# Optimization experiments

Hardware: AMD Instinct MI355X
Metric: run time of the kernel (lower is better)

The kernel has to match this reference:

```python
import jax, jax.numpy as jnp
import numpy as np

DIM = 256
NUM_HEADS = 8
WINDOW = 7


def setup_inputs() -> dict:
    key = jax.random.key(0)
    ks = jax.random.split(key, 6)
    B, N, C = 4, 2048, DIM
    x = jax.random.normal(ks[0], (B, N, C), dtype=jnp.float32)
    qkv_w = jax.random.normal(ks[1], (3 * C, C), dtype=jnp.float32) * 0.02
    qkv_b = jax.random.normal(ks[2], (3 * C,), dtype=jnp.float32) * 0.02
    proj_w = jax.random.normal(ks[3], (C, C), dtype=jnp.float32) * 0.02
    proj_b = jax.random.normal(ks[4], (C,), dtype=jnp.float32) * 0.02
    bias_table = jax.random.normal(ks[5], ((2 * WINDOW - 1) * NUM_HEADS,), dtype=jnp.float32) * 0.02
    return {"x": x, "qkv_w": qkv_w, "qkv_b": qkv_b, "proj_w": proj_w,
            "proj_b": proj_b, "bias_table": bias_table}


def _rel_bias(bias_table, seq_len):
    w = WINDOW
    coords = jnp.arange(w)
    idx = coords[:, None] - coords[None, :] + (w - 1)  # (w, w), values in [0, 2w-2]
    # Faithful to original: table[idx.view(-1)].view(w,w,-1) -> last dim 1,
    # i.e. bias is shared across heads.
    bias = bias_table[idx]  # (w, w)
    if seq_len <= w:
        return bias[:seq_len, :seq_len]
    repeats = (seq_len + w - 1) // w
    bias = jnp.tile(bias, (repeats, repeats))[:seq_len, :seq_len]
    return bias  # (N, N)


def reference(x, qkv_w, qkv_b, proj_w, proj_b, bias_table):
    B, N, C = x.shape
    H, hd = NUM_HEADS, C // NUM_HEADS
    qkv = x @ qkv_w.T + qkv_b                       # (B, N, 3C)
    qkv = qkv.reshape(B, N, 3, H, hd).transpose(2, 0, 3, 1, 4)
    q, k, v = qkv[0], qkv[1], qkv[2]                # each (B, H, N, hd)
    scale = hd ** -0.5
    attn = jnp.einsum('bhnd,bhmd->bhnm', q, k) * scale  # (B, H, N, N)
    bias = _rel_bias(bias_table, N)                 # (N, N), shared across heads
    attn = attn + bias[None, None, :, :]
    attn = jax.nn.softmax(attn, axis=-1)
    out = jnp.einsum('bhnm,bhmd->bhnd', attn, v)    # (B, H, N, hd)
    out = out.transpose(0, 2, 1, 3).reshape(B, N, C)
    return out @ proj_w.T + proj_b
```

## Files before the change

kernel.cpp:

```cpp
#include <hip/hip_runtime.h>
#include <stdint.h>

#define DIMC   256
#define NHEADS 8
#define HD     32
#define BATCH  4
#define SEQ    2048
#define MTOT   (BATCH * SEQ)
#define QKVN   (MTOT * HD * NHEADS)
#define SCALE  0.17677669529663687f
#define LOG2E  1.4426950408889634f
#define SCL2E  (SCALE * LOG2E)

typedef short bf16x8 __attribute__((ext_vector_type(8)));
typedef float f32x4  __attribute__((ext_vector_type(4)));

#if defined(__has_builtin)
#if __has_builtin(__builtin_amdgcn_exp2f)
#define EXP2F __builtin_amdgcn_exp2f
#else
#define EXP2F exp2f
#endif
#else
#define EXP2F exp2f
#endif

static __device__ __forceinline__ unsigned short f2bf(float f) {
    unsigned int u = __float_as_uint(f);
    u += 0x7fffu + ((u >> 16) & 1u);
    return (unsigned short)(u >> 16);
}

static __device__ __forceinline__ unsigned int cvt2(float a, float b) {
#if defined(__has_builtin) && __has_builtin(__builtin_amdgcn_cvt_pk_bf16_f32)
    typedef __bf16 bf2 __attribute__((ext_vector_type(2)));
    bf2 v = __builtin_amdgcn_cvt_pk_bf16_f32(a, b);
    return __builtin_bit_cast(unsigned int, v);
#else
    return (unsigned int)f2bf(a) | ((unsigned int)f2bf(b) << 16);
#endif
}

static __device__ __forceinline__ bf16x8 ld8f_bf(const float* p) {
    float4 a0 = *(const float4*)p;
    float4 a1 = *(const float4*)(p + 4);
    uint4 pk;
    pk.x = cvt2(a0.x, a0.y); pk.y = cvt2(a0.z, a0.w);
    pk.z = cvt2(a1.x, a1.y); pk.w = cvt2(a1.z, a1.w);
    return __builtin_bit_cast(bf16x8, pk);
}

__global__ __launch_bounds__(256) void gemm_qkv_kernel(
    const float* __restrict__ A,
    const float* __restrict__ W,
    const float* __restrict__ bias,
    unsigned short* __restrict__ qb,
    unsigned short* __restrict__ kb,
    unsigned short* __restrict__ vtb)
{
    __shared__ __align__(16) unsigned short FW[8][64][32];

    const int t    = threadIdx.x;
    const int wave = t >> 6;
    const int lane = t & 63;
    const int cg   = lane & 15;
    const int quad = lane >> 4;
    const int m0   = blockIdx.y * 128;
    const int n0   = blockIdx.x * 64;

    {
        int r  = t >> 2, cb = t & 3;
        int pc = (cb ^ ((r >> 1) & 3)) << 3;
        #pragma unroll
        for (int chunk = 0; chunk < 8; chunk++)
            *(bf16x8*)&FW[chunk][r][pc] =
                ld8f_bf(W + (size_t)(n0 + r) * 256 + chunk * 32 + cb * 8);
    }
    __syncthreads();

    const float* Arow = A + (size_t)(m0 + wave * 16 + cg) * 256 + quad * 8;
    const int rsw = ((cg >> 1) & 3);

    f32x4 acc[2][4];
    #pragma unroll
    for (int s = 0; s < 2; s++)
        #pragma unroll
        for (int c = 0; c < 4; c++) acc[s][c] = (f32x4){0.f, 0.f, 0.f, 0.f};

    #pragma unroll
    for (int chunk = 0; chunk < 8; chunk++) {
        bf16x8 wf[4];
        #pragma unroll
        for (int c = 0; c < 4; c++)
            wf[c] = *(const bf16x8*)&FW[chunk][c * 16 + cg][(quad ^ rsw) << 3];
        #pragma unroll
        for (int s = 0; s < 2; s++) {
            bf16x8 af = ld8f_bf(Arow + (size_t)s * 64 * 256 + chunk * 32);
            #pragma unroll
            for (int c = 0; c < 4; c++)
                acc[s][c] = __builtin_amdgcn_mfma_f32_16x16x32_bf16(af, wf[c], acc[s][c], 0, 0, 0);
        }
    }

    if (blockIdx.x >= 8) {
        float (*TR)[68] = (float (*)[68])(void*)&FW[0][0][0];
        #pragma unroll
        for (int s = 0; s < 2; s++) {
            __syncthreads();
            #pragma unroll
            for (int c = 0; c < 4; c++) {
                int l = c * 16 + cg;
                float bv = bias[n0 + l];
                float4 vv;
                vv.x = acc[s][c][0] + bv; vv.y = acc[s][c][1] + bv;
                vv.z = acc[s][c][2] + bv; vv.w = acc[s][c][3] + bv;
                *(float4*)__builtin_assume_aligned(&TR[l][wave * 16 + quad * 4], 16) = vv;
            }
            __syncthreads();
            int l  = t >> 2;
            int mm = (t & 3) << 4;
            int n  = n0 + l;
            int h  = (n >> 5) & 7;
            int d  = n & 31;
            int b_ = m0 >> 11;
            int nn = (m0 & 2047) + s * 64 + mm;
            const float* tr = (const float*)__builtin_assume_aligned(&TR[l][mm], 16);
            float4 v0 = *(const float4*)(tr);
            float4 v1 = *(const float4*)(tr + 4);
            float4 v2 = *(const float4*)(tr + 8);
            float4 v3 = *(const float4*)(tr + 12);
            uint4 pk0, pk1;
            pk0.x = cvt2(v0.x, v0.y); pk0.y = cvt2(v0.z, v0.w);
            pk0.z = cvt2(v1.x, v1.y); pk0.w = cvt2(v1.z, v1.w);
            pk1.x = cvt2(v2.x, v2.y); pk1.y = cvt2(v2.z, v2.w);
            pk1.z = cvt2(v3.x, v3.y); pk1.w = cvt2(v3.z, v3.w);
            unsigned short* dst = vtb + ((size_t)((b_ * NHEADS + h) * HD + d)) * SEQ + nn;
            *(uint4*)dst       = pk0;
            *(uint4*)(dst + 8) = pk1;
        }
        return;
    }

    #pragma unroll
    for (int s = 0; s < 2; s++) {
        #pragma unroll
        for (int c = 0; c < 4; c++) {
            int n = n0 + c * 16 + cg;
            float bv = bias[n];
            int which = n >> 8;
            int h     = (n >> 5) & 7;
            int d     = n & 31;
            #pragma unroll
            for (int rr = 0; rr < 4; rr++) {
                int m = m0 + s * 64 + wave * 16 + quad * 4 + rr;
                float val = acc[s][c][rr] + bv;
                int b_ = m >> 11;
                int nn = m & 2047;
                int bh = b_ * NHEADS + h;
                if (which == 0)
                    qb[((size_t)bh * SEQ + nn) * HD + d] = f2bf(val * SCL2E);
                else
                    kb[((size_t)bh * SEQ + nn) * HD + d] = f2bf(val);
            }
        }
    }
}

__global__ __launch_bounds__(256) void gemm_proj_kernel(
    const unsigned short* __restrict__ A,
    const float* __restrict__ W,
    const float* __restrict__ bias,
    float* __restrict__ outf)
{
    __shared__ __align__(16) unsigned short FW[8][64][32];

    const int t    = threadIdx.x;
    const int wave = t >> 6;
    const int lane = t & 63;
    const int cg   = lane & 15;
    const int quad = lane >> 4;
    const int m0   = blockIdx.y * 64;
    const int n0   = blockIdx.x * 64;

    {
        int r  = t >> 2, cb = t & 3;
        int pc = (cb ^ ((r >> 1) & 3)) << 3;
        #pragma unroll
        for (int chunk = 0; chunk < 8; chunk++)
            *(bf16x8*)&FW[chunk][r][pc] =
                ld8f_bf(W + (size_t)(n0 + r) * 256 + chunk * 32 + cb * 8);
    }
    __syncthreads();

    const unsigned short* Arow = A + (size_t)(m0 + wave * 16 + cg) * 256 + quad * 8;
    const int rsw = ((cg >> 1) & 3);

    f32x4 acc[4];
    #pragma unroll
    for (int c = 0; c < 4; c++) acc[c] = (f32x4){0.f, 0.f, 0.f, 0.f};

    #pragma unroll
    for (int chunk = 0; chunk < 8; chunk++) {
        bf16x8 af = *(const bf16x8*)(Arow + chunk * 32);
        bf16x8 wf[4];
        #pragma unroll
        for (int c = 0; c < 4; c++)
            wf[c] = *(const bf16x8*)&FW[chunk][c * 16 + cg][(quad ^ rsw) << 3];
        #pragma unroll
        for (int c = 0; c < 4; c++)
            acc[c] = __builtin_amdgcn_mfma_f32_16x16x32_bf16(af, wf[c], acc[c], 0, 0, 0);
    }

    #pragma unroll
    for (int c = 0; c < 4; c++) {
        int n = n0 + c * 16 + cg;
        float bv = bias[n];
        #pragma unroll
        for (int rr = 0; rr < 4; rr++) {
            int m = m0 + wave * 16 + quad * 4 + rr;
            outf[(size_t)m * 256 + n] = acc[c][rr] + bv;
        }
    }
}

__global__ __launch_bounds__(256) void attn_mfma_kernel(
    const unsigned short* __restrict__ Q,
    const unsigned short* __restrict__ K,
    const unsigned short* __restrict__ Vt,
    const float* __restrict__ table,
    unsigned short* __restrict__ AO)
{
    __shared__ __align__(16) unsigned short PL[4][64][72];
    __shared__ __align__(16) unsigned short KA7[7][32];

    const int t    = threadIdx.x;
    const int wave = t >> 6;
    const int lane = t & 63;
    const int cg   = lane & 15;
    const int quad = lane >> 4;

    const int bid = blockIdx.x;
    const int qt  = bid & 31;
    const int bh  = bid >> 5;
    const int b   = bh >> 3;
    const int h   = bh & 7;
    const int q0  = qt * 64;

    if (t < 224) {
        int r = t >> 5, c = t & 31;
        float v = (c < 7) ? table[c - r + 6] * LOG2E : 0.f;
        KA7[r][c] = f2bf(v);
    }
    __syncthreads();

    const unsigned short* Kbase = K  + (size_t)bh * (SEQ * HD);
    const unsigned short* Vbase = Vt + (size_t)bh * (SEQ * HD);

    bf16x8 qf[4], qfa[4];
    #pragma unroll
    for (int qi = 0; qi < 4; qi++) {
        qf[qi]  = *(const bf16x8*)(Q + (size_t)bh * (SEQ * HD) +
                                   (size_t)(q0 + qi * 16 + cg) * HD + quad * 8);
        int p = (q0 + qi * 16 + cg) % 7;
        #pragma unroll
        for (int i = 0; i < 8; i++)
            qfa[qi][i] = (quad == 0 && i == p) ? (short)0x3F80 : (short)0;
    }

    bf16x8 ones;
    #pragma unroll
    for (int i = 0; i < 8; i++) ones[i] = (short)0x3F80;

    f32x4 o[4][2], ol[4];
    #pragma unroll
    for (int qi = 0; qi < 4; qi++) {
        o[qi][0] = (f32x4){0.f, 0.f, 0.f, 0.f};
        o[qi][1] = (f32x4){0.f, 0.f, 0.f, 0.f};
        ol[qi]   = (f32x4){0.f, 0.f, 0.f, 0.f};
    }

    const int kstart = wave * (SEQ / 4);
    int kb7[4];
    #pragma unroll
    for (int jt = 0; jt < 4; jt++) kb7[jt] = (kstart + jt * 16 + cg) % 7;

    #pragma unroll 2
    for (int jj = 0; jj < SEQ / 4; jj += 64) {
        const int j0 = kstart + jj;

        bf16x8 kf[4], kfa[4];
        #pragma unroll
        for (int jt = 0; jt < 4; jt++) {
            kf[jt]  = *(const bf16x8*)(Kbase + (size_t)(j0 + jt * 16 + cg) * HD + quad * 8);
            kfa[jt] = *(const bf16x8*)&KA7[kb7[jt]][quad * 8];
        }
        bf16x8 vf[2][2];
        #pragma unroll
        for (int kt = 0; kt < 2; kt++)
            #pragma unroll
            for (int dt = 0; dt < 2; dt++)
                vf[kt][dt] = *(const bf16x8*)(Vbase + (size_t)(dt * 16 + cg) * SEQ +
                                              j0 + kt * 32 + quad * 8);

        #pragma unroll
        for (int half = 0; half < 2; half++) {
            f32x4 s[2][4];
            #pragma unroll
            for (int qh = 0; qh < 2; qh++) {
                int qi = half * 2 + qh;
                #pragma unroll
                for (int jt = 0; jt < 4; jt++) {
                    s[qh][jt] = __builtin_amdgcn_mfma_f32_16x16x32_bf16(
                        kfa[jt], qfa[qi], (f32x4){0.f, 0.f, 0.f, 0.f}, 0, 0, 0);
                    s[qh][jt] = __builtin_amdgcn_mfma_f32_16x16x32_bf16(
                        kf[jt], qf[qi], s[qh][jt], 0, 0, 0);
                }
            }
            #pragma unroll
            for (int qh = 0; qh < 2; qh++) {
                int qi = half * 2 + qh;
                #pragma unroll
                for (int jt = 0; jt < 4; jt++) {
                    float p0 = EXP2F(s[qh][jt][0]);
                    float p1 = EXP2F(s[qh][jt][1]);
                    float p2 = EXP2F(s[qh][jt][2]);
                    float p3 = EXP2F(s[qh][jt][3]);
                    uint2 w;
                    w.x = cvt2(p0, p1);
                    w.y = cvt2(p2, p3);
                    *(uint2*)&PL[wave][qi * 16 + cg][jt * 16 + quad * 4] = w;
                }
            }
        }
        __builtin_amdgcn_s_waitcnt(0xC07F);

        #pragma unroll
        for (int qi = 0; qi < 4; qi++) {
            bf16x8 pa0 = *(const bf16x8*)&PL[wave][qi * 16 + cg][quad * 8];
            bf16x8 pa1 = *(const bf16x8*)&PL[wave][qi * 16 + cg][32 + quad * 8];
            o[qi][0] = __builtin_amdgcn_mfma_f32_16x16x32_bf16(pa0, vf[0][0], o[qi][0], 0, 0, 0);
            o[qi][0] = __builtin_amdgcn_mfma_f32_16x16x32_bf16(pa1, vf[1][0], o[qi][0], 0, 0, 0);
            o[qi][1] = __builtin_amdgcn_mfma_f32_16x16x32_bf16(pa0, vf[0][1], o[qi][1], 0, 0, 0);
            o[qi][1] = __builtin_amdgcn_mfma_f32_16x16x32_bf16(pa1, vf[1][1], o[qi][1], 0, 0, 0);
            ol[qi]   = __builtin_amdgcn_mfma_f32_16x16x32_bf16(pa0, ones, ol[qi], 0, 0, 0);
            ol[qi]   = __builtin_amdgcn_mfma_f32_16x16x32_bf16(pa1, ones, ol[qi], 0, 0, 0);
        }

        #pragma unroll
        for (int jt = 0; jt < 4; jt++)
            kb7[jt] = (kb7[jt] == 6) ? 0 : kb7[jt] + 1;
    }

    __builtin_amdgcn_s_waitcnt(0xC07F);
    float* OPw = (float*)&PL[wave][0][0];
    #pragma unroll
    for (int qi = 0; qi < 4; qi++) {
        #pragma unroll
        for (int dt = 0; dt < 2; dt++)
            #pragma unroll
            for (int rr = 0; rr < 4; rr++)
                OPw[(qi * 16 + quad * 4 + rr) * 33 + dt * 16 + cg] = o[qi][dt][rr];
        if (cg == 0) {
            #pragma unroll
            for (int rr = 0; rr < 4; rr++)
                OPw[(qi * 16 + quad * 4 + rr) * 33 + 32] = ol[qi][rr];
        }
    }
    __syncthreads();

    {
        int q  = t >> 2;
        int d0 = (t & 3) << 3;
        float l = 0.f;
        float ov[8];
        #pragma unroll
        for (int i = 0; i < 8; i++) ov[i] = 0.f;
        #pragma unroll
        for (int w = 0; w < 4; w++) {
            const float* OPx = (const float*)&PL[w][0][0];
            l += OPx[q * 33 + 32];
            #pragma unroll
            for (int i = 0; i < 8; i++) ov[i] += OPx[q * 33 + d0 + i];
        }
        float inv = 1.f / l;
        unsigned short pk[8];
        #pragma unroll
        for (int i = 0; i < 8; i += 2) {
            unsigned int u = cvt2(ov[i] * inv, ov[i + 1] * inv);
            pk[i]     = (unsigned short)(u & 0xffffu);
            pk[i + 1] = (unsigned short)(u >> 16);
        }
        *(uint4*)(AO + ((size_t)(b * SEQ + q0 + q)) * DIMC + h * HD + d0) = *(const uint4*)pk;
    }
}

extern "C" void kernel_launch(void* const* d_in, const int* in_sizes, int n_in,
                              void* d_out, int out_size, void* d_ws, size_t ws_size,
                              hipStream_t stream) {
    const float* x      = (const float*)d_in[0];
    const float* qkv_w  = (const float*)d_in[1];
    const float* qkv_b  = (const float*)d_in[2];
    const float* proj_w = (const float*)d_in[3];
    const float* proj_b = (const float*)d_in[4];
    const float* table  = (const float*)d_in[5];
    float* out = (float*)d_out;

    unsigned short* ws   = (unsigned short*)d_ws;
    unsigned short* qb   = ws;
    unsigned short* kb   = qb  + (size_t)QKVN;
    unsigned short* vtb  = kb  + (size_t)QKVN;
    unsigned short* ao   = vtb + (size_t)QKVN;

    gemm_qkv_kernel<<<dim3(768 / 64, MTOT / 128), 256, 0, stream>>>(
        x, qkv_w, qkv_b, qb, kb, vtb);

    attn_mfma_kernel<<<dim3(BATCH * NHEADS * (SEQ / 64)), 256, 0, stream>>>(
        qb, kb, vtb, table, ao);

    gemm_proj_kernel<<<dim3(256 / 64, MTOT / 64), 256, 0, stream>>>(
        ao, proj_w, proj_b, out);
}
```

Before: 130.9 us.

## Widen GEMM tiles to 256 output columns per block for A reuse

Both the QKV and projection GEMMs now compute 256 output columns per block instead of 64. Each A row tile is loaded and converted once per block, rather than once per 64-column slice, which cuts redundant fp32 A reads and bf16 conversions. The cost is 128 KB of shared memory for the weight tile, a much larger accumulator register footprint, and far fewer blocks (192 and 128), which lowers occupancy and parallelism on a 256-CU device.

```diff
diff --git a/kernel.cpp b/kernel.cpp
--- a/kernel.cpp
+++ b/kernel.cpp
@@ -58,72 +58,103 @@
     unsigned short* __restrict__ kb,
     unsigned short* __restrict__ vtb)
 {
-    __shared__ __align__(16) unsigned short FW[8][64][32];
+    __shared__ __align__(16) unsigned short FW[4][8][64][32];
 
     const int t    = threadIdx.x;
     const int wave = t >> 6;
     const int lane = t & 63;
     const int cg   = lane & 15;
     const int quad = lane >> 4;
+    const int sup  = blockIdx.x;
     const int m0   = blockIdx.y * 128;
-    const int n0   = blockIdx.x * 64;
+    const int nb   = sup * 256;
 
     {
         int r  = t >> 2, cb = t & 3;
         int pc = (cb ^ ((r >> 1) & 3)) << 3;
         #pragma unroll
-        for (int chunk = 0; chunk < 8; chunk++)
-            *(bf16x8*)&FW[chunk][r][pc] =
-                ld8f_bf(W + (size_t)(n0 + r) * 256 + chunk * 32 + cb * 8);
+        for (int nt = 0; nt < 4; nt++)
+            #pragma unroll
+            for (int chunk = 0; chunk < 8; chunk++)
+                *(bf16x8*)&FW[nt][chunk][r][pc] =
+                    ld8f_bf(W + (size_t)(nb + nt * 64 + r) * 256 + chunk * 32 + cb * 8);
     }
     __syncthreads();
 
     const float* Arow = A + (size_t)(m0 + wave * 16 + cg) * 256 + quad * 8;
     const int rsw = ((cg >> 1) & 3);
 
-    f32x4 acc[2][4];
+    f32x4 acc[2][4][4];
     #pragma unroll
     for (int s = 0; s < 2; s++)
         #pragma unroll
-        for (int c = 0; c < 4; c++) acc[s][c] = (f32x4){0.f, 0.f, 0.f, 0.f};
+        for (int nt = 0; nt < 4; nt++)
+            #pragma unroll
+            for (int c = 0; c < 4; c++) acc[s][nt][c] = (f32x4){0.f, 0.f, 0.f, 0.f};
 
     #pragma unroll
     for (int chunk = 0; chunk < 8; chunk++) {
-        bf16x8 wf[4];
-        #pragma unroll
-        for (int c = 0; c < 4; c++)
-            wf[c] = *(const bf16x8*)&FW[chunk][c * 16 + cg][(quad ^ rsw) << 3];
-        #pragma unroll
-        for (int s = 0; s < 2; s++) {
-            bf16x8 af = ld8f_bf(Arow + (size_t)s * 64 * 256 + chunk * 32);
-            #pragma unroll
-            for (int c = 0; c < 4; c++)
-                acc[s][c] = __builtin_amdgcn_mfma_f32_16x16x32_bf16(af, wf[c], acc[s][c], 0, 0, 0);
-        }
-    }
-
-    if (blockIdx.x >= 8) {
-        float (*TR)[68] = (float (*)[68])(void*)&FW[0][0][0];
+        bf16x8 af[2];
+        #pragma unroll
+        for (int s = 0; s < 2; s++)
+            af[s] = ld8f_bf(Arow + (size_t)s * 64 * 256 + chunk * 32);
+        #pragma unroll
+        for (int nt = 0; nt < 4; nt++)
+            #pragma unroll
+            for (int c = 0; c < 4; c++) {
+                bf16x8 wf = *(const bf16x8*)&FW[nt][chunk][c * 16 + cg][(quad ^ rsw) << 3];
+                #pragma unroll
+                for (int s = 0; s < 2; s++)
+                    acc[s][nt][c] = __builtin_amdgcn_mfma_f32_16x16x32_bf16(
+                        af[s], wf, acc[s][nt][c], 0, 0, 0);
+            }
+    }
+
+    if (sup < 2) {
+        unsigned short* dstb = (sup == 0) ? qb : kb;
+        float scl = (sup == 0) ? SCL2E : 1.0f;
+        #pragma unroll
+        for (int s = 0; s < 2; s++)
+            #pragma unroll
+            for (int nt = 0; nt < 4; nt++)
+                #pragma unroll
+                for (int c = 0; c < 4; c++) {
+                    int nl = nt * 64 + c * 16 + cg;
+                    float bv = bias[nb + nl];
+                    int h = nl >> 5, d = nl & 31;
+                    #pragma unroll
+                    for (int rr = 0; rr < 4; rr++) {
+                        int m  = m0 + s * 64 + wave * 16 + quad * 4 + rr;
+                        int b_ = m >> 11, nn = m & 2047;
+                        dstb[((size_t)(b_ * NHEADS + h) * SEQ + nn) * HD + d] =
+                            f2bf((acc[s][nt][c][rr] + bv) * scl);
+                    }
+                }
+        return;
+    }
+
+    float (*TR)[68] = (float (*)[68])(void*)&FW[0][0][0][0];
+    #pragma unroll
+    for (int nt = 0; nt < 4; nt++) {
         #pragma unroll
         for (int s = 0; s < 2; s++) {
             __syncthreads();
             #pragma unroll
             for (int c = 0; c < 4; c++) {
                 int l = c * 16 + cg;
-                float bv = bias[n0 + l];
+                float bv = bias[nb + nt * 64 + l];
                 float4 vv;
-                vv.x = acc[s][c][0] + bv; vv.y = acc[s][c][1] + bv;
-                vv.z = acc[s][c][2] + bv; vv.w = acc[s][c][3] + bv;
+                vv.x = acc[s][nt][c][0] + bv; vv.y = acc[s][nt][c][1] + bv;
+                vv.z = acc[s][nt][c][2] + bv; vv.w = acc[s][nt][c][3] + bv;
                 *(float4*)__builtin_assume_aligned(&TR[l][wave * 16 + quad * 4], 16) = vv;
             }
             __syncthreads();
             int l  = t >> 2;
             int mm = (t & 3) << 4;
-            int n  = n0 + l;
-            int h  = (n >> 5) & 7;
-            int d  = n & 31;
-            int b_ = m0 >> 11;
-            int nn = (m0 & 2047) + s * 64 + mm;
+            int nl = nt * 64 + l;
+            int h  = nl >> 5, d = nl & 31;
+            int m  = m0 + s * 64 + mm;
+            int b_ = m >> 11, nn = m & 2047;
             const float* tr = (const float*)__builtin_assume_aligned(&TR[l][mm], 16);
             float4 v0 = *(const float4*)(tr);
             float4 v1 = *(const float4*)(tr + 4);
@@ -138,31 +169,6 @@
             *(uint4*)dst       = pk0;
             *(uint4*)(dst + 8) = pk1;
         }
-        return;
-    }
-
-    #pragma unroll
-    for (int s = 0; s < 2; s++) {
-        #pragma unroll
-        for (int c = 0; c < 4; c++) {
-            int n = n0 + c * 16 + cg;
-            float bv = bias[n];
-            int which = n >> 8;
-            int h     = (n >> 5) & 7;
-            int d     = n & 31;
-            #pragma unroll
-            for (int rr = 0; rr < 4; rr++) {
-                int m = m0 + s * 64 + wave * 16 + quad * 4 + rr;
-                float val = acc[s][c][rr] + bv;
-                int b_ = m >> 11;
-                int nn = m & 2047;
-                int bh = b_ * NHEADS + h;
-                if (which == 0)
-                    qb[((size_t)bh * SEQ + nn) * HD + d] = f2bf(val * SCL2E);
-                else
-                    kb[((size_t)bh * SEQ + nn) * HD + d] = f2bf(val);
-            }
-        }
     }
 }
 
@@ -172,7 +178,7 @@
     const float* __restrict__ bias,
     float* __restrict__ outf)
 {
-    __shared__ __align__(16) unsigned short FW[8][64][32];
+    __shared__ __align__(16) unsigned short FW[4][8][64][32];
 
     const int t    = threadIdx.x;
     const int wave = t >> 6;
@@ -180,47 +186,52 @@
     const int cg   = lane & 15;
     const int quad = lane >> 4;
     const int m0   = blockIdx.y * 64;
-    const int n0   = blockIdx.x * 64;
 
     {
         int r  = t >> 2, cb = t & 3;
         int pc = (cb ^ ((r >> 1) & 3)) << 3;
         #pragma unroll
-        for (int chunk = 0; chunk < 8; chunk++)
-            *(bf16x8*)&FW[chunk][r][pc] =
-                ld8f_bf(W + (size_t)(n0 + r) * 256 + chunk * 32 + cb * 8);
+        for (int nt = 0; nt < 4; nt++)
+            #pragma unroll
+            for (int chunk = 0; chunk < 8; chunk++)
+                *(bf16x8*)&FW[nt][chunk][r][pc] =
+                    ld8f_bf(W + (size_t)(nt * 64 + r) * 256 + chunk * 32 + cb * 8);
     }
     __syncthreads();
 
     const unsigned short* Arow = A + (size_t)(m0 + wave * 16 + cg) * 256 + quad * 8;
     const int rsw = ((cg >> 1) & 3);
 
-    f32x4 acc[4];
-    #pragma unroll
-    for (int c = 0; c < 4; c++) acc[c] = (f32x4){0.f, 0.f, 0.f, 0.f};
+    f32x4 acc[4][4];
+    #pragma unroll
+    for (int nt = 0; nt < 4; nt++)
+        #pragma unroll
+        for (int c = 0; c < 4; c++) acc[nt][c] = (f32x4){0.f, 0.f, 0.f, 0.f};
 
     #pragma unroll
     for (int chunk = 0; chunk < 8; chunk++) {
         bf16x8 af = *(const bf16x8*)(Arow + chunk * 32);
-        bf16x8 wf[4];
-        #pragma unroll
-        for (int c = 0; c < 4; c++)
-            wf[c] = *(const bf16x8*)&FW[chunk][c * 16 + cg][(quad ^ rsw) << 3];
-        #pragma unroll
-        for (int c = 0; c < 4; c++)
-            acc[c] = __builtin_amdgcn_mfma_f32_16x16x32_bf16(af, wf[c], acc[c], 0, 0, 0);
-    }
-
-    #pragma unroll
-    for (int c = 0; c < 4; c++) {
-        int n = n0 + c * 16 + cg;
-        float bv = bias[n];
-        #pragma unroll
-        for (int rr = 0; rr < 4; rr++) {
-            int m = m0 + wave * 16 + quad * 4 + rr;
-            outf[(size_t)m * 256 + n] = acc[c][rr] + bv;
-        }
-    }
+        #pragma unroll
+        for (int nt = 0; nt < 4; nt++)
+            #pragma unroll
+            for (int c = 0; c < 4; c++) {
+                bf16x8 wf = *(const bf16x8*)&FW[nt][chunk][c * 16 + cg][(quad ^ rsw) << 3];
+                acc[nt][c] = __builtin_amdgcn_mfma_f32_16x16x32_bf16(af, wf, acc[nt][c], 0, 0, 0);
+            }
+    }
+
+    #pragma unroll
+    for (int nt = 0; nt < 4; nt++)
+        #pragma unroll
+        for (int c = 0; c < 4; c++) {
+            int n = nt * 64 + c * 16 + cg;
+            float bv = bias[n];
+            #pragma unroll
+            for (int rr = 0; rr < 4; rr++) {
+                int m = m0 + wave * 16 + quad * 4 + rr;
+                outf[(size_t)m * 256 + n] = acc[nt][c][rr] + bv;
+            }
+        }
 }
 
 __global__ __launch_bounds__(256) void attn_mfma_kernel(
@@ -411,12 +422,12 @@
     unsigned short* vtb  = kb  + (size_t)QKVN;
     unsigned short* ao   = vtb + (size_t)QKVN;
 
-    gemm_qkv_kernel<<<dim3(768 / 64, MTOT / 128), 256, 0, stream>>>(
+    gemm_qkv_kernel<<<dim3(3, 64), 256, 0, stream>>>(
         x, qkv_w, qkv_b, qb, kb, vtb);
 
     attn_mfma_kernel<<<dim3(BATCH * NHEADS * (SEQ / 64)), 256, 0, stream>>>(
         qb, kb, vtb, table, ao);
 
-    gemm_proj_kernel<<<dim3(256 / 64, MTOT / 64), 256, 0, stream>>>(
+    gemm_proj_kernel<<<dim3(1, 128), 256, 0, stream>>>(
         ao, proj_w, proj_b, out);
 }
```

After: 136.1 us. 4.0% more time.

## Shrink shared memory footprints in GEMM and attention kernels for occupancy

Applied to the files above, without the earlier changes.

The QKV and projection GEMMs now stage the weight tile in two halves of four K-chunks each, halving their weight LDS buffer at the cost of an extra barrier per block. The attention kernel shrinks its per-wave P buffer to 32 rows with an XOR swizzle instead of padding, runs the PV MFMAs after each half rather than once per tile, and does the cross-wave reduction in two passes of 32 rows. The aim is lower LDS use per block so more blocks fit per CU, traded against extra synchronization and more waitcnt stalls between the softmax and PV stages.

```diff
diff --git a/kernel.cpp b/kernel.cpp
--- a/kernel.cpp
+++ b/kernel.cpp
@@ -58,7 +58,9 @@
     unsigned short* __restrict__ kb,
     unsigned short* __restrict__ vtb)
 {
-    __shared__ __align__(16) unsigned short FW[8][64][32];
+    __shared__ __align__(16) unsigned char SM[17408];
+    unsigned short (*FW)[64][32] = (unsigned short (*)[64][32])SM;
+    float (*TR)[68] = (float (*)[68])SM;
 
     const int t    = threadIdx.x;
     const int wave = t >> 6;
@@ -68,16 +70,6 @@
     const int m0   = blockIdx.y * 128;
     const int n0   = blockIdx.x * 64;
 
-    {
-        int r  = t >> 2, cb = t & 3;
-        int pc = (cb ^ ((r >> 1) & 3)) << 3;
-        #pragma unroll
-        for (int chunk = 0; chunk < 8; chunk++)
-            *(bf16x8*)&FW[chunk][r][pc] =
-                ld8f_bf(W + (size_t)(n0 + r) * 256 + chunk * 32 + cb * 8);
-    }
-    __syncthreads();
-
     const float* Arow = A + (size_t)(m0 + wave * 16 + cg) * 256 + quad * 8;
     const int rsw = ((cg >> 1) & 3);
 
@@ -88,22 +80,36 @@
         for (int c = 0; c < 4; c++) acc[s][c] = (f32x4){0.f, 0.f, 0.f, 0.f};
 
     #pragma unroll
-    for (int chunk = 0; chunk < 8; chunk++) {
-        bf16x8 wf[4];
-        #pragma unroll
-        for (int c = 0; c < 4; c++)
-            wf[c] = *(const bf16x8*)&FW[chunk][c * 16 + cg][(quad ^ rsw) << 3];
-        #pragma unroll
-        for (int s = 0; s < 2; s++) {
-            bf16x8 af = ld8f_bf(Arow + (size_t)s * 64 * 256 + chunk * 32);
+    for (int half = 0; half < 2; half++) {
+        if (half) __syncthreads();
+        {
+            int r  = t >> 2, cb = t & 3;
+            int pc = (cb ^ ((r >> 1) & 3)) << 3;
+            #pragma unroll
+            for (int c4 = 0; c4 < 4; c4++)
+                *(bf16x8*)&FW[c4][r][pc] =
+                    ld8f_bf(W + (size_t)(n0 + r) * 256 + (half * 4 + c4) * 32 + cb * 8);
+        }
+        __syncthreads();
+
+        #pragma unroll
+        for (int c4 = 0; c4 < 4; c4++) {
+            int chunk = half * 4 + c4;
+            bf16x8 wf[4];
             #pragma unroll
             for (int c = 0; c < 4; c++)
-                acc[s][c] = __builtin_amdgcn_mfma_f32_16x16x32_bf16(af, wf[c], acc[s][c], 0, 0, 0);
+                wf[c] = *(const bf16x8*)&FW[c4][c * 16 + cg][(quad ^ rsw) << 3];
+            #pragma unroll
+            for (int s = 0; s < 2; s++) {
+                bf16x8 af = ld8f_bf(Arow + (size_t)s * 64 * 256 + chunk * 32);
+                #pragma unroll
+                for (int c = 0; c < 4; c++)
+                    acc[s][c] = __builtin_amdgcn_mfma_f32_16x16x32_bf16(af, wf[c], acc[s][c], 0, 0, 0);
+            }
         }
     }
 
     if (blockIdx.x >= 8) {
-        float (*TR)[68] = (float (*)[68])(void*)&FW[0][0][0];
         #pragma unroll
         for (int s = 0; s < 2; s++) {
             __syncthreads();
@@ -172,7 +178,7 @@
     const float* __restrict__ bias,
     float* __restrict__ outf)
 {
-    __shared__ __align__(16) unsigned short FW[8][64][32];
+    __shared__ __align__(16) unsigned short FW[4][64][32];
 
     const int t    = threadIdx.x;
     const int wave = t >> 6;
@@ -182,16 +188,6 @@
     const int m0   = blockIdx.y * 64;
     const int n0   = blockIdx.x * 64;
 
-    {
-        int r  = t >> 2, cb = t & 3;
-        int pc = (cb ^ ((r >> 1) & 3)) << 3;
-        #pragma unroll
-        for (int chunk = 0; chunk < 8; chunk++)
-            *(bf16x8*)&FW[chunk][r][pc] =
-                ld8f_bf(W + (size_t)(n0 + r) * 256 + chunk * 32 + cb * 8);
-    }
-    __syncthreads();
-
     const unsigned short* Arow = A + (size_t)(m0 + wave * 16 + cg) * 256 + quad * 8;
     const int rsw = ((cg >> 1) & 3);
 
@@ -200,15 +196,30 @@
     for (int c = 0; c < 4; c++) acc[c] = (f32x4){0.f, 0.f, 0.f, 0.f};
 
     #pragma unroll
-    for (int chunk = 0; chunk < 8; chunk++) {
-        bf16x8 af = *(const bf16x8*)(Arow + chunk * 32);
-        bf16x8 wf[4];
-        #pragma unroll
-        for (int c = 0; c < 4; c++)
-            wf[c] = *(const bf16x8*)&FW[chunk][c * 16 + cg][(quad ^ rsw) << 3];
-        #pragma unroll
-        for (int c = 0; c < 4; c++)
-            acc[c] = __builtin_amdgcn_mfma_f32_16x16x32_bf16(af, wf[c], acc[c], 0, 0, 0);
+    for (int half = 0; half < 2; half++) {
+        if (half) __syncthreads();
+        {
+            int r  = t >> 2, cb = t & 3;
+            int pc = (cb ^ ((r >> 1) & 3)) << 3;
+            #pragma unroll
+            for (int c4 = 0; c4 < 4; c4++)
+                *(bf16x8*)&FW[c4][r][pc] =
+                    ld8f_bf(W + (size_t)(n0 + r) * 256 + (half * 4 + c4) * 32 + cb * 8);
+        }
+        __syncthreads();
+
+        #pragma unroll
+        for (int c4 = 0; c4 < 4; c4++) {
+            int chunk = half * 4 + c4;
+            bf16x8 af = *(const bf16x8*)(Arow + chunk * 32);
+            bf16x8 wf[4];
+            #pragma unroll
+            for (int c = 0; c < 4; c++)
+                wf[c] = *(const bf16x8*)&FW[c4][c * 16 + cg][(quad ^ rsw) << 3];
+            #pragma unroll
+            for (int c = 0; c < 4; c++)
+                acc[c] = __builtin_amdgcn_mfma_f32_16x16x32_bf16(af, wf[c], acc[c], 0, 0, 0);
+        }
     }
 
     #pragma unroll
@@ -230,7 +241,7 @@
     const float* __restrict__ table,
     unsigned short* __restrict__ AO)
 {
-    __shared__ __align__(16) unsigned short PL[4][64][72];
+    __shared__ __align__(16) unsigned char SMEM[4][4224];
     __shared__ __align__(16) unsigned short KA7[7][32];
 
     const int t    = threadIdx.x;
@@ -255,6 +266,8 @@
 
     const unsigned short* Kbase = K  + (size_t)bh * (SEQ * HD);
     const unsigned short* Vbase = Vt + (size_t)bh * (SEQ * HD);
+    unsigned short* Pw = (unsigned short*)&SMEM[wave][0];
+    const int csw = cg & 7;
 
     bf16x8 qf[4], qfa[4];
     #pragma unroll
@@ -318,7 +331,6 @@
             }
             #pragma unroll
             for (int qh = 0; qh < 2; qh++) {
-                int qi = half * 2 + qh;
                 #pragma unroll
                 for (int jt = 0; jt < 4; jt++) {
                     float p0 = EXP2F(s[qh][jt][0]);
@@ -328,22 +340,24 @@
                     uint2 w;
                     w.x = cvt2(p0, p1);
                     w.y = cvt2(p2, p3);
-                    *(uint2*)&PL[wave][qi * 16 + cg][jt * 16 + quad * 4] = w;
+                    int pc = (2 * jt + (quad >> 1)) ^ csw;
+                    *(uint2*)(Pw + (qh * 16 + cg) * 64 + pc * 8 + (quad & 1) * 4) = w;
                 }
             }
-        }
-        __builtin_amdgcn_s_waitcnt(0xC07F);
-
-        #pragma unroll
-        for (int qi = 0; qi < 4; qi++) {
-            bf16x8 pa0 = *(const bf16x8*)&PL[wave][qi * 16 + cg][quad * 8];
-            bf16x8 pa1 = *(const bf16x8*)&PL[wave][qi * 16 + cg][32 + quad * 8];
-            o[qi][0] = __builtin_amdgcn_mfma_f32_16x16x32_bf16(pa0, vf[0][0], o[qi][0], 0, 0, 0);
-            o[qi][0] = __builtin_amdgcn_mfma_f32_16x16x32_bf16(pa1, vf[1][0], o[qi][0], 0, 0, 0);
-            o[qi][1] = __builtin_amdgcn_mfma_f32_16x16x32_bf16(pa0, vf[0][1], o[qi][1], 0, 0, 0);
-            o[qi][1] = __builtin_amdgcn_mfma_f32_16x16x32_bf16(pa1, vf[1][1], o[qi][1], 0, 0, 0);
-            ol[qi]   = __builtin_amdgcn_mfma_f32_16x16x32_bf16(pa0, ones, ol[qi], 0, 0, 0);
-            ol[qi]   = __builtin_amdgcn_mfma_f32_16x16x32_bf16(pa1, ones, ol[qi], 0, 0, 0);
+            __builtin_amdgcn_s_waitcnt(0xC07F);
+
+            #pragma unroll
+            for (int qh = 0; qh < 2; qh++) {
+                int qi = half * 2 + qh;
+                bf16x8 pa0 = *(const bf16x8*)(Pw + (qh * 16 + cg) * 64 + ((quad ^ csw) << 3));
+                bf16x8 pa1 = *(const bf16x8*)(Pw + (qh * 16 + cg) * 64 + (((4 + quad) ^ csw) << 3));
+                o[qi][0] = __builtin_amdgcn_mfma_f32_16x16x32_bf16(pa0, vf[0][0], o[qi][0], 0, 0, 0);
+                o[qi][0] = __builtin_amdgcn_mfma_f32_16x16x32_bf16(pa1, vf[1][0], o[qi][0], 0, 0, 0);
+                o[qi][1] = __builtin_amdgcn_mfma_f32_16x16x32_bf16(pa0, vf[0][1], o[qi][1], 0, 0, 0);
+                o[qi][1] = __builtin_amdgcn_mfma_f32_16x16x32_bf16(pa1, vf[1][1], o[qi][1], 0, 0, 0);
+                ol[qi]   = __builtin_amdgcn_mfma_f32_16x16x32_bf16(pa0, ones, ol[qi], 0, 0, 0);
+                ol[qi]   = __builtin_amdgcn_mfma_f32_16x16x32_bf16(pa1, ones, ol[qi], 0, 0, 0);
+            }
         }
 
         #pragma unroll
@@ -351,46 +365,41 @@
             kb7[jt] = (kb7[jt] == 6) ? 0 : kb7[jt] + 1;
     }
 
-    __builtin_amdgcn_s_waitcnt(0xC07F);
-    float* OPw = (float*)&PL[wave][0][0];
-    #pragma unroll
-    for (int qi = 0; qi < 4; qi++) {
-        #pragma unroll
-        for (int dt = 0; dt < 2; dt++)
-            #pragma unroll
-            for (int rr = 0; rr < 4; rr++)
-                OPw[(qi * 16 + quad * 4 + rr) * 33 + dt * 16 + cg] = o[qi][dt][rr];
-        if (cg == 0) {
-            #pragma unroll
-            for (int rr = 0; rr < 4; rr++)
-                OPw[(qi * 16 + quad * 4 + rr) * 33 + 32] = ol[qi][rr];
-        }
-    }
-    __syncthreads();
-
-    {
-        int q  = t >> 2;
-        int d0 = (t & 3) << 3;
+    #pragma unroll
+    for (int p = 0; p < 2; p++) {
+        __syncthreads();
+        float* OPw = (float*)&SMEM[wave][0];
+        #pragma unroll
+        for (int qh = 0; qh < 2; qh++) {
+            int qi = p * 2 + qh;
+            #pragma unroll
+            for (int dt = 0; dt < 2; dt++)
+                #pragma unroll
+                for (int rr = 0; rr < 4; rr++)
+                    OPw[(qh * 16 + quad * 4 + rr) * 33 + dt * 16 + cg] = o[qi][dt][rr];
+            if (cg == 0) {
+                #pragma unroll
+                for (int rr = 0; rr < 4; rr++)
+                    OPw[(qh * 16 + quad * 4 + rr) * 33 + 32] = ol[qi][rr];
+            }
+        }
+        __syncthreads();
+        int ql = t >> 3;
+        int d0 = (t & 7) << 2;
         float l = 0.f;
-        float ov[8];
-        #pragma unroll
-        for (int i = 0; i < 8; i++) ov[i] = 0.f;
+        float ov[4] = {0.f, 0.f, 0.f, 0.f};
         #pragma unroll
         for (int w = 0; w < 4; w++) {
-            const float* OPx = (const float*)&PL[w][0][0];
-            l += OPx[q * 33 + 32];
-            #pragma unroll
-            for (int i = 0; i < 8; i++) ov[i] += OPx[q * 33 + d0 + i];
+            const float* OPx = (const float*)&SMEM[w][0];
+            l += OPx[ql * 33 + 32];
+            #pragma unroll
+            for (int i = 0; i < 4; i++) ov[i] += OPx[ql * 33 + d0 + i];
         }
         float inv = 1.f / l;
-        unsigned short pk[8];
-        #pragma unroll
-        for (int i = 0; i < 8; i += 2) {
-            unsigned int u = cvt2(ov[i] * inv, ov[i + 1] * inv);
-            pk[i]     = (unsigned short)(u & 0xffffu);
-            pk[i + 1] = (unsigned short)(u >> 16);
-        }
-        *(uint4*)(AO + ((size_t)(b * SEQ + q0 + q)) * DIMC + h * HD + d0) = *(const uint4*)pk;
+        uint2 pk;
+        pk.x = cvt2(ov[0] * inv, ov[1] * inv);
+        pk.y = cvt2(ov[2] * inv, ov[3] * inv);
+        *(uint2*)(AO + ((size_t)(b * SEQ + q0 + p * 32 + ql)) * DIMC + h * HD + d0) = pk;
     }
 }
 
@@ -411,12 +420,12 @@
     unsigned short* vtb  = kb  + (size_t)QKVN;
     unsigned short* ao   = vtb + (size_t)QKVN;
 
-    gemm_qkv_kernel<<<dim3(768 / 64, MTOT / 128), 256, 0, stream>>>(
+    gemm_qkv_kernel<<<dim3(12, 64), 256, 0, stream>>>(
         x, qkv_w, qkv_b, qb, kb, vtb);
 
     attn_mfma_kernel<<<dim3(BATCH * NHEADS * (SEQ / 64)), 256, 0, stream>>>(
         qb, kb, vtb, table, ao);
 
-    gemm_proj_kernel<<<dim3(256 / 64, MTOT / 64), 256, 0, stream>>>(
+    gemm_proj_kernel<<<dim3(4, 128), 256, 0, stream>>>(
         ao, proj_w, proj_b, out);
 }
```

New measurement: 154.2 us. 1.18x slower.

## Hold weight fragments in registers and drop LDS staging in both GEMMs

Applied to the files above, without the earlier changes.

Both projection GEMMs stop staging the weight tile in shared memory. Each wave instead keeps its 16 output columns' weight fragments in registers for the whole K=256 and reuses them across 128 rows, loading A fragments straight from global. The V transpose now writes packed uint2 directly instead of going through an LDS transpose. The proj kernel processes 128 rows per block, so the grid is halved, and the KA7 LDS row is padded to 40. This removes LDS traffic and barriers but increases redundant global A loads per block, since each wave re-reads all A rows, and raises register pressure.

```diff
diff --git a/kernel.cpp b/kernel.cpp
--- a/kernel.cpp
+++ b/kernel.cpp
@@ -58,109 +58,70 @@
     unsigned short* __restrict__ kb,
     unsigned short* __restrict__ vtb)
 {
-    __shared__ __align__(16) unsigned short FW[8][64][32];
-
     const int t    = threadIdx.x;
     const int wave = t >> 6;
     const int lane = t & 63;
     const int cg   = lane & 15;
     const int quad = lane >> 4;
-    const int m0   = blockIdx.y * 128;
     const int n0   = blockIdx.x * 64;
-
-    {
-        int r  = t >> 2, cb = t & 3;
-        int pc = (cb ^ ((r >> 1) & 3)) << 3;
-        #pragma unroll
-        for (int chunk = 0; chunk < 8; chunk++)
-            *(bf16x8*)&FW[chunk][r][pc] =
-                ld8f_bf(W + (size_t)(n0 + r) * 256 + chunk * 32 + cb * 8);
-    }
-    __syncthreads();
-
-    const float* Arow = A + (size_t)(m0 + wave * 16 + cg) * 256 + quad * 8;
-    const int rsw = ((cg >> 1) & 3);
-
-    f32x4 acc[2][4];
-    #pragma unroll
-    for (int s = 0; s < 2; s++)
-        #pragma unroll
-        for (int c = 0; c < 4; c++) acc[s][c] = (f32x4){0.f, 0.f, 0.f, 0.f};
-
-    #pragma unroll
-    for (int chunk = 0; chunk < 8; chunk++) {
-        bf16x8 wf[4];
-        #pragma unroll
-        for (int c = 0; c < 4; c++)
-            wf[c] = *(const bf16x8*)&FW[chunk][c * 16 + cg][(quad ^ rsw) << 3];
-        #pragma unroll
-        for (int s = 0; s < 2; s++) {
-            bf16x8 af = ld8f_bf(Arow + (size_t)s * 64 * 256 + chunk * 32);
-            #pragma unroll
-            for (int c = 0; c < 4; c++)
-                acc[s][c] = __builtin_amdgcn_mfma_f32_16x16x32_bf16(af, wf[c], acc[s][c], 0, 0, 0);
-        }
-    }
-
-    if (blockIdx.x >= 8) {
-        float (*TR)[68] = (float (*)[68])(void*)&FW[0][0][0];
-        #pragma unroll
-        for (int s = 0; s < 2; s++) {
-            __syncthreads();
-            #pragma unroll
-            for (int c = 0; c < 4; c++) {
-                int l = c * 16 + cg;
-                float bv = bias[n0 + l];
-                float4 vv;
-                vv.x = acc[s][c][0] + bv; vv.y = acc[s][c][1] + bv;
-                vv.z = acc[s][c][2] + bv; vv.w = acc[s][c][3] + bv;
-                *(float4*)__builtin_assume_aligned(&TR[l][wave * 16 + quad * 4], 16) = vv;
-            }
-            __syncthreads();
-            int l  = t >> 2;
-            int mm = (t & 3) << 4;
-            int n  = n0 + l;
-            int h  = (n >> 5) & 7;
-            int d  = n & 31;
-            int b_ = m0 >> 11;
-            int nn = (m0 & 2047) + s * 64 + mm;
-            const float* tr = (const float*)__builtin_assume_aligned(&TR[l][mm], 16);
-            float4 v0 = *(const float4*)(tr);
-            float4 v1 = *(const float4*)(tr + 4);
-            float4 v2 = *(const float4*)(tr + 8);
-            float4 v3 = *(const float4*)(tr + 12);
-            uint4 pk0, pk1;
-            pk0.x = cvt2(v0.x, v0.y); pk0.y = cvt2(v0.z, v0.w);
-            pk0.z = cvt2(v1.x, v1.y); pk0.w = cvt2(v1.z, v1.w);
-            pk1.x = cvt2(v2.x, v2.y); pk1.y = cvt2(v2.z, v2.w);
-            pk1.z = cvt2(v3.x, v3.y); pk1.w = cvt2(v3.z, v3.w);
-            unsigned short* dst = vtb + ((size_t)((b_ * NHEADS + h) * HD + d)) * SEQ + nn;
-            *(uint4*)dst       = pk0;
-            *(uint4*)(dst + 8) = pk1;
-        }
-        return;
-    }
-
-    #pragma unroll
-    for (int s = 0; s < 2; s++) {
-        #pragma unroll
-        for (int c = 0; c < 4; c++) {
-            int n = n0 + c * 16 + cg;
-            float bv = bias[n];
-            int which = n >> 8;
-            int h     = (n >> 5) & 7;
-            int d     = n & 31;
-            #pragma unroll
-            for (int rr = 0; rr < 4; rr++) {
-                int m = m0 + s * 64 + wave * 16 + quad * 4 + rr;
-                float val = acc[s][c][rr] + bv;
-                int b_ = m >> 11;
-                int nn = m & 2047;
-                int bh = b_ * NHEADS + h;
-                if (which == 0)
-                    qb[((size_t)bh * SEQ + nn) * HD + d] = f2bf(val * SCL2E);
-                else
-                    kb[((size_t)bh * SEQ + nn) * HD + d] = f2bf(val);
+    const int mg   = blockIdx.y * 128;
+
+    const int n = n0 + wave * 16 + cg;
+    bf16x8 wf[8];
+    #pragma unroll
+    for (int chunk = 0; chunk < 8; chunk++)
+        wf[chunk] = ld8f_bf(W + (size_t)n * 256 + chunk * 32 + quad * 8);
+
+    const int which = n >> 8;
+    const int h     = (n >> 5) & 7;
+    const int d     = n & 31;
+    const float bv  = bias[n];
+
+    #pragma unroll
+    for (int l = 0; l < 2; l++) {
+        const int m0l = mg + l * 64;
+        const float* Ab = A + (size_t)m0l * 256;
+
+        f32x4 acc[4];
+        #pragma unroll
+        for (int mi = 0; mi < 4; mi++) acc[mi] = (f32x4){0.f, 0.f, 0.f, 0.f};
+
+        #pragma unroll
+        for (int chunk = 0; chunk < 8; chunk++) {
+            #pragma unroll
+            for (int mi = 0; mi < 4; mi++) {
+                bf16x8 af = ld8f_bf(Ab + (size_t)(mi * 16 + cg) * 256 + chunk * 32 + quad * 8);
+                acc[mi] = __builtin_amdgcn_mfma_f32_16x16x32_bf16(af, wf[chunk], acc[mi], 0, 0, 0);
+            }
+        }
+
+        const int b_ = m0l >> 11;
+        const int bh = b_ * NHEADS + h;
+        if (which == 0) {
+            #pragma unroll
+            for (int mi = 0; mi < 4; mi++)
+                #pragma unroll
+                for (int rr = 0; rr < 4; rr++) {
+                    int nn = (m0l & 2047) + mi * 16 + quad * 4 + rr;
+                    qb[((size_t)bh * SEQ + nn) * HD + d] = f2bf((acc[mi][rr] + bv) * SCL2E);
+                }
+        } else if (which == 1) {
+            #pragma unroll
+            for (int mi = 0; mi < 4; mi++)
+                #pragma unroll
+                for (int rr = 0; rr < 4; rr++) {
+                    int nn = (m0l & 2047) + mi * 16 + quad * 4 + rr;
+                    kb[((size_t)bh * SEQ + nn) * HD + d] = f2bf(acc[mi][rr] + bv);
+                }
+        } else {
+            unsigned short* vrow = vtb + ((size_t)bh * HD + d) * SEQ;
+            #pragma unroll
+            for (int mi = 0; mi < 4; mi++) {
+                int nn = (m0l & 2047) + mi * 16 + quad * 4;
+                uint2 pk;
+                pk.x = cvt2(acc[mi][0] + bv, acc[mi][1] + bv);
+                pk.y = cvt2(acc[mi][2] + bv, acc[mi][3] + bv);
+                *(uint2*)(vrow + nn) = pk;
             }
         }
     }
@@ -172,54 +133,46 @@
     const float* __restrict__ bias,
     float* __restrict__ outf)
 {
-    __shared__ __align__(16) unsigned short FW[8][64][32];
-
     const int t    = threadIdx.x;
     const int wave = t >> 6;
     const int lane = t & 63;
     const int cg   = lane & 15;
     const int quad = lane >> 4;
-    const int m0   = blockIdx.y * 64;
     const int n0   = blockIdx.x * 64;
-
-    {
-        int r  = t >> 2, cb = t & 3;
-        int pc = (cb ^ ((r >> 1) & 3)) << 3;
-        #pragma unroll
-        for (int chunk = 0; chunk < 8; chunk++)
-            *(bf16x8*)&FW[chunk][r][pc] =
-                ld8f_bf(W + (size_t)(n0 + r) * 256 + chunk * 32 + cb * 8);
-    }
-    __syncthreads();
-
-    const unsigned short* Arow = A + (size_t)(m0 + wave * 16 + cg) * 256 + quad * 8;
-    const int rsw = ((cg >> 1) & 3);
-
-    f32x4 acc[4];
-    #pragma unroll
-    for (int c = 0; c < 4; c++) acc[c] = (f32x4){0.f, 0.f, 0.f, 0.f};
-
-    #pragma unroll
-    for (int chunk = 0; chunk < 8; chunk++) {
-        bf16x8 af = *(const bf16x8*)(Arow + chunk * 32);
-        bf16x8 wf[4];
-        #pragma unroll
-        for (int c = 0; c < 4; c++)
-            wf[c] = *(const bf16x8*)&FW[chunk][c * 16 + cg][(quad ^ rsw) << 3];
-        #pragma unroll
-        for (int c = 0; c < 4; c++)
-            acc[c] = __builtin_amdgcn_mfma_f32_16x16x32_bf16(af, wf[c], acc[c], 0, 0, 0);
-    }
-
-    #pragma unroll
-    for (int c = 0; c < 4; c++) {
-        int n = n0 + c * 16 + cg;
-        float bv = bias[n];
-        #pragma unroll
-        for (int rr = 0; rr < 4; rr++) {
-            int m = m0 + wave * 16 + quad * 4 + rr;
-            outf[(size_t)m * 256 + n] = acc[c][rr] + bv;
-        }
+    const int mg   = blockIdx.y * 128;
+
+    const int n = n0 + wave * 16 + cg;
+    bf16x8 wf[8];
+    #pragma unroll
+    for (int chunk = 0; chunk < 8; chunk++)
+        wf[chunk] = ld8f_bf(W + (size_t)n * 256 + chunk * 32 + quad * 8);
+    const float bv = bias[n];
+
+    #pragma unroll
+    for (int l = 0; l < 2; l++) {
+        const int m0l = mg + l * 64;
+        const unsigned short* Ab = A + (size_t)m0l * 256;
+
+        f32x4 acc[4];
+        #pragma unroll
+        for (int mi = 0; mi < 4; mi++) acc[mi] = (f32x4){0.f, 0.f, 0.f, 0.f};
+
+        #pragma unroll
+        for (int chunk = 0; chunk < 8; chunk++) {
+            #pragma unroll
+            for (int mi = 0; mi < 4; mi++) {
+                bf16x8 af = *(const bf16x8*)(Ab + (size_t)(mi * 16 + cg) * 256 + chunk * 32 + quad * 8);
+                acc[mi] = __builtin_amdgcn_mfma_f32_16x16x32_bf16(af, wf[chunk], acc[mi], 0, 0, 0);
+            }
+        }
+
+        #pragma unroll
+        for (int mi = 0; mi < 4; mi++)
+            #pragma unroll
+            for (int rr = 0; rr < 4; rr++) {
+                int m = m0l + mi * 16 + quad * 4 + rr;
+                outf[(size_t)m * 256 + n] = acc[mi][rr] + bv;
+            }
     }
 }
 
@@ -231,7 +184,7 @@
     unsigned short* __restrict__ AO)
 {
     __shared__ __align__(16) unsigned short PL[4][64][72];
-    __shared__ __align__(16) unsigned short KA7[7][32];
+    __shared__ __align__(16) unsigned short KA7[7][40];
 
     const int t    = threadIdx.x;
     const int wave = t >> 6;
@@ -411,12 +364,12 @@
     unsigned short* vtb  = kb  + (size_t)QKVN;
     unsigned short* ao   = vtb + (size_t)QKVN;
 
-    gemm_qkv_kernel<<<dim3(768 / 64, MTOT / 128), 256, 0, stream>>>(
+    gemm_qkv_kernel<<<dim3(12, 64), 256, 0, stream>>>(
         x, qkv_w, qkv_b, qb, kb, vtb);
 
     attn_mfma_kernel<<<dim3(BATCH * NHEADS * (SEQ / 64)), 256, 0, stream>>>(
         qb, kb, vtb, table, ao);
 
-    gemm_proj_kernel<<<dim3(256 / 64, MTOT / 64), 256, 0, stream>>>(
+    gemm_proj_kernel<<<dim3(4, 64), 256, 0, stream>>>(
         ao, proj_w, proj_b, out);
 }
```

After: 167.9 us. +28.3%, slower.
